# Kernel tuning notes

Measured on AMD Instinct MI355X. Metric: run time of the kernel, lower is better.

Reference implementation:

```python
import jax, jax.numpy as jnp
import numpy as np

B = 32          # batch (num decoding sequences)
H = 32          # query heads
KVH = 8         # kv heads (GQA)
HD = 128        # head dim
BS = 16         # kv-cache block size
MAX_KV = 4096   # max kv length per sequence
BLOCKS_PER_SEQ = MAX_KV // BS
NB = B * BLOCKS_PER_SEQ  # total cache blocks
SCALE = 1.0 / float(np.sqrt(HD))


def setup_inputs() -> dict:
    key = jax.random.key(0)
    k1, k2, k3, k4 = jax.random.split(key, 4)
    q = jax.random.normal(k1, (B, H, HD), dtype=jnp.float32)
    k_cache = jax.random.normal(k2, (NB, BS, KVH, HD), dtype=jnp.float32)
    v_cache = jax.random.normal(k3, (NB, BS, KVH, HD), dtype=jnp.float32)
    # at least 1 valid token per sequence
    cache_seqlens = jax.random.randint(k4, (B,), 1, MAX_KV + 1, dtype=jnp.int32)
    # each sequence owns a contiguous, distinct set of blocks
    block_tables = jnp.arange(NB, dtype=jnp.int32).reshape(B, BLOCKS_PER_SEQ)
    return {"q": q, "k_cache": k_cache, "v_cache": v_cache,
            "cache_seqlens": cache_seqlens, "block_tables": block_tables}


def reference(q, k_cache, v_cache, cache_seqlens, block_tables):
    # Gather paged KV blocks per sequence: [B, BLOCKS, BS, KVH, HD] -> [B, S, KVH, HD]
    k = k_cache[block_tables].reshape(B, MAX_KV, KVH, HD)
    v = v_cache[block_tables].reshape(B, MAX_KV, KVH, HD)
    g = H // KVH  # query heads per kv head
    qg = q.reshape(B, KVH, g, HD)
    # scores: [B, KVH, g, S]
    scores = jnp.einsum('bkgd,bskd->bkgs', qg, k) * SCALE
    # mask out positions beyond cache_seqlens (causal with q_len=1 reduces to length mask)
    valid = jnp.arange(MAX_KV)[None, :] < cache_seqlens[:, None]  # [B, S]
    neg = jnp.finfo(scores.dtype).min
    scores = jnp.where(valid[:, None, None, :], scores, neg)
    p = jax.nn.softmax(scores, axis=-1)
    out = jnp.einsum('bkgs,bskd->bkgd', p, v).reshape(B, H, HD)
    return out
```

## Files before the change

kernel.cpp:

```cpp
#include <hip/hip_runtime.h>
#include <math.h>

#define NB_B 32
#define NH 32
#define NKVH 8
#define GQ 4
#define HD 128
#define BS 16
#define MAX_KV 4096
#define BPS 256
#define NSPLIT 4
#define SPLIT_LEN 1024
#define ATT_SCALE 0.08838834764831845f

__device__ __forceinline__ float wave_max64(float v) {
#pragma unroll
  for (int off = 32; off > 0; off >>= 1) v = fmaxf(v, __shfl_xor(v, off, 64));
  return v;
}
__device__ __forceinline__ float wave_sum64(float v) {
#pragma unroll
  for (int off = 32; off > 0; off >>= 1) v += __shfl_xor(v, off, 64);
  return v;
}

__launch_bounds__(256, 2)
__global__ void attn_split_kernel(const float* __restrict__ q,
                                  const float* __restrict__ kc,
                                  const float* __restrict__ vc,
                                  const int* __restrict__ seqlens,
                                  const int* __restrict__ btab,
                                  float* __restrict__ ws_o,
                                  float* __restrict__ ws_m,
                                  float* __restrict__ ws_l) {
  const int split = blockIdx.x;
  const int kvh   = blockIdx.y;
  const int b     = blockIdx.z;
  const int tid   = threadIdx.x;
  const int wave  = tid >> 6;
  const int lane  = tid & 63;

  const int seqlen = seqlens[b];
  const int start  = split * SPLIT_LEN;
  const int end    = min(seqlen, start + SPLIT_LEN);
  const int midx   = ((b * NKVH + kvh) * NSPLIT + split) * GQ;

  if (end <= start) {
    if (tid < GQ) { ws_m[midx + tid] = -INFINITY; ws_l[midx + tid] = 0.f; }
    float* op = ws_o + (size_t)midx * HD;
    op[tid] = 0.f;
    op[tid + 256] = 0.f;
    return;
  }

  __shared__ float p_lds[4][GQ][64];
  __shared__ float wm[4][GQ];
  __shared__ float wl[4][GQ];
  __shared__ float wo[4][GQ][HD];

  float m_h[GQ], lpart[GQ];
  float2 o2[GQ];
#pragma unroll
  for (int h = 0; h < GQ; ++h) {
    m_h[h] = -INFINITY;
    lpart[h] = 0.f;
    o2[h] = make_float2(0.f, 0.f);
  }

  const float* qbase = q + ((size_t)b * NH + (size_t)kvh * GQ) * HD;
  const int* bt = btab + (size_t)b * BPS;

#pragma unroll 1
  for (int cbase = start + wave * 64; cbase < end; cbase += 4 * 64) {
    const int tok = cbase + lane;
    const int blk = bt[tok >> 4];
    const float* krow = kc + (((size_t)blk * BS + (tok & 15)) * NKVH + kvh) * HD;

    float s[GQ] = {0.f, 0.f, 0.f, 0.f};
#pragma unroll
    for (int dg = 0; dg < HD; dg += 4) {
      const float4 k4 = *(const float4*)(krow + dg);
#pragma unroll
      for (int h = 0; h < GQ; ++h) {
        const float* qh = qbase + h * HD + dg;
        s[h] = fmaf(qh[0], k4.x, s[h]);
        s[h] = fmaf(qh[1], k4.y, s[h]);
        s[h] = fmaf(qh[2], k4.z, s[h]);
        s[h] = fmaf(qh[3], k4.w, s[h]);
      }
    }

    const bool valid = (tok < end);
#pragma unroll
    for (int h = 0; h < GQ; ++h) {
      const float sv = valid ? s[h] * ATT_SCALE : -INFINITY;
      const float mx = wave_max64(sv);
      const float mnew = fmaxf(m_h[h], mx);
      const float alpha = __expf(m_h[h] - mnew);
      const float p = __expf(sv - mnew);
      m_h[h] = mnew;
      lpart[h] = lpart[h] * alpha + p;
      o2[h].x *= alpha;
      o2[h].y *= alpha;
      p_lds[wave][h][lane] = p;
    }
    __builtin_amdgcn_wave_barrier();

#pragma unroll
    for (int blk4 = 0; blk4 < 4; ++blk4) {
      const int t0 = cbase + blk4 * 16;
      const int pblk = bt[t0 >> 4];
      const float* vbase = vc + ((size_t)pblk * BS * NKVH + kvh) * HD;
#pragma unroll
      for (int tt = 0; tt < 16; tt += 4) {
        float2 vv[4];
#pragma unroll
        for (int j = 0; j < 4; ++j)
          vv[j] = *(const float2*)(vbase + (size_t)(tt + j) * NKVH * HD + 2 * lane);
#pragma unroll
        for (int h = 0; h < GQ; ++h) {
          const float4 pq = *(const float4*)&p_lds[wave][h][blk4 * 16 + tt];
          o2[h].x = fmaf(pq.x, vv[0].x, o2[h].x);
          o2[h].y = fmaf(pq.x, vv[0].y, o2[h].y);
          o2[h].x = fmaf(pq.y, vv[1].x, o2[h].x);
          o2[h].y = fmaf(pq.y, vv[1].y, o2[h].y);
          o2[h].x = fmaf(pq.z, vv[2].x, o2[h].x);
          o2[h].y = fmaf(pq.z, vv[2].y, o2[h].y);
          o2[h].x = fmaf(pq.w, vv[3].x, o2[h].x);
          o2[h].y = fmaf(pq.w, vv[3].y, o2[h].y);
        }
      }
    }
  }

#pragma unroll
  for (int h = 0; h < GQ; ++h) {
    const float ls = wave_sum64(lpart[h]);
    if (lane == 0) { wm[wave][h] = m_h[h]; wl[wave][h] = ls; }
    wo[wave][h][2 * lane]     = o2[h].x;
    wo[wave][h][2 * lane + 1] = o2[h].y;
  }
  __syncthreads();

  const int h  = tid >> 6;
  const int dp = tid & 63;
  const float M = fmaxf(fmaxf(wm[0][h], wm[1][h]), fmaxf(wm[2][h], wm[3][h]));
  float L = 0.f, ox = 0.f, oy = 0.f;
#pragma unroll
  for (int w = 0; w < 4; ++w) {
    const float f = __expf(wm[w][h] - M);
    L  += wl[w][h] * f;
    ox += wo[w][h][2 * dp] * f;
    oy += wo[w][h][2 * dp + 1] * f;
  }
  const size_t oidx = (size_t)(midx + h) * HD;
  ws_o[oidx + 2 * dp]     = ox;
  ws_o[oidx + 2 * dp + 1] = oy;
  if (dp == 0) { ws_m[midx + h] = M; ws_l[midx + h] = L; }
}

__global__ void attn_combine_kernel(const float* __restrict__ ws_o,
                                    const float* __restrict__ ws_m,
                                    const float* __restrict__ ws_l,
                                    float* __restrict__ out) {
  const int bh = blockIdx.x;
  const int b  = bh / NH;
  const int hg = bh % NH;
  const int kvh = hg / GQ;
  const int h   = hg % GQ;
  const int d = threadIdx.x;
  const int base = ((b * NKVH + kvh) * NSPLIT) * GQ + h;

  float M = -INFINITY;
#pragma unroll
  for (int s = 0; s < NSPLIT; ++s) M = fmaxf(M, ws_m[base + s * GQ]);
  float L = 0.f, acc = 0.f;
#pragma unroll
  for (int s = 0; s < NSPLIT; ++s) {
    const float f = __expf(ws_m[base + s * GQ] - M);
    L   += ws_l[base + s * GQ] * f;
    acc += ws_o[(size_t)(base + s * GQ) * HD + d] * f;
  }
  out[(size_t)bh * HD + d] = acc / L;
}

extern "C" void kernel_launch(void* const* d_in, const int* in_sizes, int n_in,
                              void* d_out, int out_size, void* d_ws, size_t ws_size,
                              hipStream_t stream) {
  const float* q       = (const float*)d_in[0];
  const float* kc      = (const float*)d_in[1];
  const float* vc      = (const float*)d_in[2];
  const int*   seqlens = (const int*)d_in[3];
  const int*   btab    = (const int*)d_in[4];
  float* out = (float*)d_out;

  float* ws_o = (float*)d_ws;
  float* ws_m = ws_o + (size_t)NB_B * NKVH * NSPLIT * GQ * HD;
  float* ws_l = ws_m + (size_t)NB_B * NKVH * NSPLIT * GQ;

  dim3 grid1(NSPLIT, NKVH, NB_B);
  attn_split_kernel<<<grid1, 256, 0, stream>>>(q, kc, vc, seqlens, btab, ws_o, ws_m, ws_l);
  attn_combine_kernel<<<NB_B * NH, 128, 0, stream>>>(ws_o, ws_m, ws_l, out);
}
```

Measured before the change: 1.033 ms.

## Use 16 splits with one 64-token chunk per wave and float4 V loads

Raises the split count from 4 to 16 so each wave handles exactly one 64-token chunk, which removes the online-softmax loop and its rescaling. Splits that start past the sequence length now exit early, and the combine kernel reads only the splits that exist. The PV product now has each lane load float4 of V across two token parities, with a shuffle reduction at the end, and occupancy is raised to four blocks per SM. The goals are better load balance and more memory parallelism across the ragged sequence lengths. The costs are a much larger grid with more partial outputs to combine, and tighter register limits from the occupancy hint.

```diff
diff --git a/kernel.cpp b/kernel.cpp
--- a/kernel.cpp
+++ b/kernel.cpp
@@ -9,8 +9,8 @@
 #define BS 16
 #define MAX_KV 4096
 #define BPS 256
-#define NSPLIT 4
-#define SPLIT_LEN 1024
+#define NSPLIT 16
+#define SPLIT_LEN 256
 #define ATT_SCALE 0.08838834764831845f
 
 __device__ __forceinline__ float wave_max64(float v) {
@@ -24,7 +24,7 @@
   return v;
 }
 
-__launch_bounds__(256, 2)
+__launch_bounds__(256, 4)
 __global__ void attn_split_kernel(const float* __restrict__ q,
                                   const float* __restrict__ kc,
                                   const float* __restrict__ vc,
@@ -42,39 +42,35 @@
 
   const int seqlen = seqlens[b];
   const int start  = split * SPLIT_LEN;
-  const int end    = min(seqlen, start + SPLIT_LEN);
-  const int midx   = ((b * NKVH + kvh) * NSPLIT + split) * GQ;
-
-  if (end <= start) {
-    if (tid < GQ) { ws_m[midx + tid] = -INFINITY; ws_l[midx + tid] = 0.f; }
-    float* op = ws_o + (size_t)midx * HD;
-    op[tid] = 0.f;
-    op[tid + 256] = 0.f;
-    return;
-  }
-
-  __shared__ float p_lds[4][GQ][64];
+  if (start >= seqlen) return;
+  const int end  = min(seqlen, start + SPLIT_LEN);
+  const int midx = ((b * NKVH + kvh) * NSPLIT + split) * GQ;
+
+  __shared__ float p_par[4][GQ][64];
   __shared__ float wm[4][GQ];
   __shared__ float wl[4][GQ];
   __shared__ float wo[4][GQ][HD];
 
-  float m_h[GQ], lpart[GQ];
-  float2 o2[GQ];
+  const float* qbase = q + ((size_t)b * NH + (size_t)kvh * GQ) * HD;
+  const int* bt = btab + (size_t)b * BPS;
+
+  const int cbase = start + wave * 64;
+  const bool wvalid = (cbase < end);
+
+  float m_h[GQ], l_h[GQ];
+  float4 o4[GQ];
 #pragma unroll
   for (int h = 0; h < GQ; ++h) {
     m_h[h] = -INFINITY;
-    lpart[h] = 0.f;
-    o2[h] = make_float2(0.f, 0.f);
-  }
-
-  const float* qbase = q + ((size_t)b * NH + (size_t)kvh * GQ) * HD;
-  const int* bt = btab + (size_t)b * BPS;
-
-#pragma unroll 1
-  for (int cbase = start + wave * 64; cbase < end; cbase += 4 * 64) {
+    l_h[h] = 0.f;
+    o4[h] = make_float4(0.f, 0.f, 0.f, 0.f);
+  }
+
+  if (wvalid) {
     const int tok = cbase + lane;
+    const bool valid = (tok < end);
     const int blk = bt[tok >> 4];
-    const float* krow = kc + (((size_t)blk * BS + (tok & 15)) * NKVH + kvh) * HD;
+    const float* krow = kc + (((size_t)blk * BS + (tok & (BS - 1))) * NKVH + kvh) * HD;
 
     float s[GQ] = {0.f, 0.f, 0.f, 0.f};
 #pragma unroll
@@ -90,55 +86,71 @@
       }
     }
 
-    const bool valid = (tok < end);
 #pragma unroll
     for (int h = 0; h < GQ; ++h) {
       const float sv = valid ? s[h] * ATT_SCALE : -INFINITY;
-      const float mx = wave_max64(sv);
-      const float mnew = fmaxf(m_h[h], mx);
-      const float alpha = __expf(m_h[h] - mnew);
-      const float p = __expf(sv - mnew);
-      m_h[h] = mnew;
-      lpart[h] = lpart[h] * alpha + p;
-      o2[h].x *= alpha;
-      o2[h].y *= alpha;
-      p_lds[wave][h][lane] = p;
+      const float m  = wave_max64(sv);
+      const float p  = __expf(sv - m);
+      m_h[h] = m;
+      l_h[h] = wave_sum64(p);
+      p_par[wave][h][(lane & 1) * 32 + (lane >> 1)] = p;
     }
     __builtin_amdgcn_wave_barrier();
 
+    const int d4 = (lane & 31) * 4;
+    const int tp = lane >> 5;
 #pragma unroll
     for (int blk4 = 0; blk4 < 4; ++blk4) {
       const int t0 = cbase + blk4 * 16;
-      const int pblk = bt[t0 >> 4];
-      const float* vbase = vc + ((size_t)pblk * BS * NKVH + kvh) * HD;
-#pragma unroll
-      for (int tt = 0; tt < 16; tt += 4) {
-        float2 vv[4];
-#pragma unroll
-        for (int j = 0; j < 4; ++j)
-          vv[j] = *(const float2*)(vbase + (size_t)(tt + j) * NKVH * HD + 2 * lane);
-#pragma unroll
-        for (int h = 0; h < GQ; ++h) {
-          const float4 pq = *(const float4*)&p_lds[wave][h][blk4 * 16 + tt];
-          o2[h].x = fmaf(pq.x, vv[0].x, o2[h].x);
-          o2[h].y = fmaf(pq.x, vv[0].y, o2[h].y);
-          o2[h].x = fmaf(pq.y, vv[1].x, o2[h].x);
-          o2[h].y = fmaf(pq.y, vv[1].y, o2[h].y);
-          o2[h].x = fmaf(pq.z, vv[2].x, o2[h].x);
-          o2[h].y = fmaf(pq.z, vv[2].y, o2[h].y);
-          o2[h].x = fmaf(pq.w, vv[3].x, o2[h].x);
-          o2[h].y = fmaf(pq.w, vv[3].y, o2[h].y);
+      if (t0 < end) {
+        const int pblk = bt[t0 >> 4];
+        const float* vbase = vc + ((size_t)pblk * BS * NKVH + kvh) * HD;
+#pragma unroll
+        for (int ttg = 0; ttg < 16; ttg += 8) {
+          float4 vv[4];
+#pragma unroll
+          for (int j = 0; j < 4; ++j)
+            vv[j] = *(const float4*)(vbase + (size_t)(ttg + tp + 2 * j) * (NKVH * HD) + d4);
+#pragma unroll
+          for (int h = 0; h < GQ; ++h) {
+            const float4 pq = *(const float4*)&p_par[wave][h][tp * 32 + blk4 * 8 + (ttg >> 1)];
+            o4[h].x = fmaf(pq.x, vv[0].x, o4[h].x);
+            o4[h].y = fmaf(pq.x, vv[0].y, o4[h].y);
+            o4[h].z = fmaf(pq.x, vv[0].z, o4[h].z);
+            o4[h].w = fmaf(pq.x, vv[0].w, o4[h].w);
+            o4[h].x = fmaf(pq.y, vv[1].x, o4[h].x);
+            o4[h].y = fmaf(pq.y, vv[1].y, o4[h].y);
+            o4[h].z = fmaf(pq.y, vv[1].z, o4[h].z);
+            o4[h].w = fmaf(pq.y, vv[1].w, o4[h].w);
+            o4[h].x = fmaf(pq.z, vv[2].x, o4[h].x);
+            o4[h].y = fmaf(pq.z, vv[2].y, o4[h].y);
+            o4[h].z = fmaf(pq.z, vv[2].z, o4[h].z);
+            o4[h].w = fmaf(pq.z, vv[2].w, o4[h].w);
+            o4[h].x = fmaf(pq.w, vv[3].x, o4[h].x);
+            o4[h].y = fmaf(pq.w, vv[3].y, o4[h].y);
+            o4[h].z = fmaf(pq.w, vv[3].z, o4[h].z);
+            o4[h].w = fmaf(pq.w, vv[3].w, o4[h].w);
+          }
         }
       }
     }
-  }
-
-#pragma unroll
-  for (int h = 0; h < GQ; ++h) {
-    const float ls = wave_sum64(lpart[h]);
-    if (lane == 0) { wm[wave][h] = m_h[h]; wl[wave][h] = ls; }
-    wo[wave][h][2 * lane]     = o2[h].x;
-    wo[wave][h][2 * lane + 1] = o2[h].y;
+
+#pragma unroll
+    for (int h = 0; h < GQ; ++h) {
+      o4[h].x += __shfl_xor(o4[h].x, 32, 64);
+      o4[h].y += __shfl_xor(o4[h].y, 32, 64);
+      o4[h].z += __shfl_xor(o4[h].z, 32, 64);
+      o4[h].w += __shfl_xor(o4[h].w, 32, 64);
+    }
+  }
+
+  if (lane == 0) {
+#pragma unroll
+    for (int h = 0; h < GQ; ++h) { wm[wave][h] = m_h[h]; wl[wave][h] = l_h[h]; }
+  }
+  if (lane < 32) {
+#pragma unroll
+    for (int h = 0; h < GQ; ++h) *(float4*)&wo[wave][h][4 * lane] = o4[h];
   }
   __syncthreads();
 
@@ -162,6 +174,7 @@
 __global__ void attn_combine_kernel(const float* __restrict__ ws_o,
                                     const float* __restrict__ ws_m,
                                     const float* __restrict__ ws_l,
+                                    const int* __restrict__ seqlens,
                                     float* __restrict__ out) {
   const int bh = blockIdx.x;
   const int b  = bh / NH;
@@ -169,14 +182,13 @@
   const int kvh = hg / GQ;
   const int h   = hg % GQ;
   const int d = threadIdx.x;
+  const int nsp = (seqlens[b] + SPLIT_LEN - 1) / SPLIT_LEN;
   const int base = ((b * NKVH + kvh) * NSPLIT) * GQ + h;
 
   float M = -INFINITY;
-#pragma unroll
-  for (int s = 0; s < NSPLIT; ++s) M = fmaxf(M, ws_m[base + s * GQ]);
+  for (int s = 0; s < nsp; ++s) M = fmaxf(M, ws_m[base + s * GQ]);
   float L = 0.f, acc = 0.f;
-#pragma unroll
-  for (int s = 0; s < NSPLIT; ++s) {
+  for (int s = 0; s < nsp; ++s) {
     const float f = __expf(ws_m[base + s * GQ] - M);
     L   += ws_l[base + s * GQ] * f;
     acc += ws_o[(size_t)(base + s * GQ) * HD + d] * f;
@@ -200,5 +212,5 @@
 
   dim3 grid1(NSPLIT, NKVH, NB_B);
   attn_split_kernel<<<grid1, 256, 0, stream>>>(q, kc, vc, seqlens, btab, ws_o, ws_m, ws_l);
-  attn_combine_kernel<<<NB_B * NH, 128, 0, stream>>>(ws_o, ws_m, ws_l, out);
-}
+  attn_combine_kernel<<<NB_B * NH, 128, 0, stream>>>(ws_o, ws_m, ws_l, seqlens, out);
+}
```

Result: faster. 968.7 us (-6.2%).
